# Kernel optimization log

Measured on AMD Instinct MI355X. Metric: run time of the kernel, lower is better.

## Reference

```python
import jax, jax.numpy as jnp
import numpy as np

DECAY = 0.95

def setup_inputs() -> dict:
    key = jax.random.key(0)
    k1, k2, k3, k4 = jax.random.split(key, 4)
    B, S, H, Dk, Dv = 4, 4096, 16, 64, 64
    return {
        "memory": jax.random.normal(k1, (H, Dk, Dv), dtype=jnp.float32),
        "keys": jax.random.normal(k2, (B, S, H, Dk), dtype=jnp.float32),
        "values": jax.random.normal(k3, (B, S, H, Dv), dtype=jnp.float32),
        "write_strengths": jax.random.uniform(k4, (B, S), dtype=jnp.float32),
    }

def reference(memory, keys, values, write_strengths):
    # M_new = decay * M + sum_{b,s} rho[b,s] * k[b,s,h] v[b,s,h]^T
    # Algebraically equivalent to per-head (rho-weighted) K^T V contraction;
    # avoids materializing the (B,S,H,Dk,Dv) outer-product tensor.
    delta = jnp.einsum('bs,bshk,bshv->hkv', write_strengths, keys, values)
    return DECAY * memory + delta
```

## Files before the change

kernel.cpp:

```cpp
#include <hip/hip_runtime.h>

constexpr int HH   = 16;
constexpr int DK   = 64;
constexpr int DV   = 64;
constexpr int ROWS = 16384;
constexpr int TS   = 32;
constexpr int NCHUNK = 64;
constexpr int RPC  = ROWS / NCHUNK;
constexpr int NT   = RPC / TS;
constexpr float DECAY = 0.95f;

__global__ __launch_bounds__(256) void init_out(const float* __restrict__ mem,
                                                float* __restrict__ out) {
    int i = blockIdx.x * blockDim.x + threadIdx.x;
    out[i] = DECAY * mem[i];
}

__global__ __launch_bounds__(256) void accum(const float* __restrict__ keys,
                                             const float* __restrict__ values,
                                             const float* __restrict__ rho,
                                             float* __restrict__ out) {
    __shared__ float sK[2][TS * DK];
    __shared__ float sV[2][TS * DV];

    const int t     = threadIdx.x;
    const int chunk = blockIdx.x;
    const int h     = blockIdx.y;

    const int tv = t & 15;
    const int tk = t >> 4;

    const int srow = t >> 4;
    const int sc4  = (t & 15) * 4;

    float acc[4][4] = {{0.f}};

    const int base_row = chunk * RPC;

    float4 kA, kB, vA, vB;

    {
        int rA = base_row + srow;
        int rB = rA + 16;
        kA = *(const float4*)(keys   + (rA * HH + h) * DK + sc4);
        kB = *(const float4*)(keys   + (rB * HH + h) * DK + sc4);
        vA = *(const float4*)(values + (rA * HH + h) * DV + sc4);
        vB = *(const float4*)(values + (rB * HH + h) * DV + sc4);
        float wA = rho[rA], wB = rho[rB];
        kA.x *= wA; kA.y *= wA; kA.z *= wA; kA.w *= wA;
        kB.x *= wB; kB.y *= wB; kB.z *= wB; kB.w *= wB;
        *(float4*)&sK[0][srow * DK + sc4]        = kA;
        *(float4*)&sK[0][(srow + 16) * DK + sc4] = kB;
        *(float4*)&sV[0][srow * DV + sc4]        = vA;
        *(float4*)&sV[0][(srow + 16) * DV + sc4] = vB;
    }
    __syncthreads();

    for (int tile = 0; tile < NT; ++tile) {
        const int cur  = tile & 1;
        const int nxt  = cur ^ 1;
        const bool more = (tile + 1) < NT;

        if (more) {
            int rA = base_row + (tile + 1) * TS + srow;
            int rB = rA + 16;
            kA = *(const float4*)(keys   + (rA * HH + h) * DK + sc4);
            kB = *(const float4*)(keys   + (rB * HH + h) * DK + sc4);
            vA = *(const float4*)(values + (rA * HH + h) * DV + sc4);
            vB = *(const float4*)(values + (rB * HH + h) * DV + sc4);
            float wA = rho[rA], wB = rho[rB];
            kA.x *= wA; kA.y *= wA; kA.z *= wA; kA.w *= wA;
            kB.x *= wB; kB.y *= wB; kB.z *= wB; kB.w *= wB;
        }

        const float* kb = sK[cur];
        const float* vb = sV[cur];
        #pragma unroll
        for (int s = 0; s < TS; ++s) {
            float4 kf = *(const float4*)(kb + s * DK + tk * 4);
            float4 vf = *(const float4*)(vb + s * DV + tv * 4);
            acc[0][0] = fmaf(kf.x, vf.x, acc[0][0]);
            acc[0][1] = fmaf(kf.x, vf.y, acc[0][1]);
            acc[0][2] = fmaf(kf.x, vf.z, acc[0][2]);
            acc[0][3] = fmaf(kf.x, vf.w, acc[0][3]);
            acc[1][0] = fmaf(kf.y, vf.x, acc[1][0]);
            acc[1][1] = fmaf(kf.y, vf.y, acc[1][1]);
            acc[1][2] = fmaf(kf.y, vf.z, acc[1][2]);
            acc[1][3] = fmaf(kf.y, vf.w, acc[1][3]);
            acc[2][0] = fmaf(kf.z, vf.x, acc[2][0]);
            acc[2][1] = fmaf(kf.z, vf.y, acc[2][1]);
            acc[2][2] = fmaf(kf.z, vf.z, acc[2][2]);
            acc[2][3] = fmaf(kf.z, vf.w, acc[2][3]);
            acc[3][0] = fmaf(kf.w, vf.x, acc[3][0]);
            acc[3][1] = fmaf(kf.w, vf.y, acc[3][1]);
            acc[3][2] = fmaf(kf.w, vf.z, acc[3][2]);
            acc[3][3] = fmaf(kf.w, vf.w, acc[3][3]);
        }
        __syncthreads();
        if (more) {
            *(float4*)&sK[nxt][srow * DK + sc4]        = kA;
            *(float4*)&sK[nxt][(srow + 16) * DK + sc4] = kB;
            *(float4*)&sV[nxt][srow * DV + sc4]        = vA;
            *(float4*)&sV[nxt][(srow + 16) * DV + sc4] = vB;
        }
        __syncthreads();
    }

    float* red = &sK[0][0];
    #pragma unroll
    for (int i = 0; i < 4; ++i)
        #pragma unroll
        for (int j = 0; j < 4; ++j)
            red[(tk * 4 + i) * DV + tv * 4 + j] = acc[i][j];
    __syncthreads();

    float* o = out + h * (DK * DV);
    #pragma unroll
    for (int i = 0; i < 16; ++i)
        atomicAdd(o + i * 256 + t, red[i * 256 + t]);
}

extern "C" void kernel_launch(void* const* d_in, const int* in_sizes, int n_in,
                              void* d_out, int out_size, void* d_ws, size_t ws_size,
                              hipStream_t stream) {
    const float* mem    = (const float*)d_in[0];
    const float* keys   = (const float*)d_in[1];
    const float* values = (const float*)d_in[2];
    const float* rho    = (const float*)d_in[3];
    float* out = (float*)d_out;

    init_out<<<dim3((HH * DK * DV) / 256), dim3(256), 0, stream>>>(mem, out);

    dim3 grid(NCHUNK, HH);
    accum<<<grid, dim3(256), 0, stream>>>(keys, values, rho, out);
}
```

Before: 164.7 us.

## Give each wavefront its own row slice with 8x8 register tiles

Each of the four wavefronts now handles a private quarter of the block's rows, with its own double-buffered LDS tiles. This removes the block-wide barriers from the main loop. Each thread now computes the full 64x64 outer product as an 8x8 register tile, which doubles FMAs per LDS load. The four per-wave partial sums are reduced in shared memory before the atomic adds. The cost is many more accumulator registers (64 per thread), and the new launch-bound hint could force spills.

```diff
diff --git a/kernel.cpp b/kernel.cpp
--- a/kernel.cpp
+++ b/kernel.cpp
@@ -1,123 +1,152 @@
 #include <hip/hip_runtime.h>
 
-constexpr int HH   = 16;
-constexpr int DK   = 64;
-constexpr int DV   = 64;
+
+constexpr int HH = 16;
+constexpr int DK = 64;
+constexpr int DV = 64;
 constexpr int ROWS = 16384;
-constexpr int TS   = 32;
 constexpr int NCHUNK = 64;
-constexpr int RPC  = ROWS / NCHUNK;
-constexpr int NT   = RPC / TS;
+constexpr int RPB = ROWS / NCHUNK;
+constexpr int RPW = RPB / 4;
+constexpr int TR = 8;
+constexpr int NT = RPW / TR;
 constexpr float DECAY = 0.95f;
 
 __global__ __launch_bounds__(256) void init_out(const float* __restrict__ mem,
                                                 float* __restrict__ out) {
-    int i = blockIdx.x * blockDim.x + threadIdx.x;
+    int i = blockIdx.x * 256 + threadIdx.x;
     out[i] = DECAY * mem[i];
 }
 
-__global__ __launch_bounds__(256) void accum(const float* __restrict__ keys,
-                                             const float* __restrict__ values,
-                                             const float* __restrict__ rho,
-                                             float* __restrict__ out) {
-    __shared__ float sK[2][TS * DK];
-    __shared__ float sV[2][TS * DV];
+__global__ __launch_bounds__(256, 4) void accum(const float* __restrict__ keys,
+                                                const float* __restrict__ values,
+                                                const float* __restrict__ rho,
+                                                float* __restrict__ out) {
+    __shared__ float smem[8192];
 
-    const int t     = threadIdx.x;
+    const int t    = threadIdx.x;
+    const int w    = t >> 6;
+    const int lane = t & 63;
+    const int tk   = lane >> 3;
+    const int tv   = lane & 7;
     const int chunk = blockIdx.x;
     const int h     = blockIdx.y;
 
-    const int tv = t & 15;
-    const int tk = t >> 4;
+    float* kb = smem + w * 1024;
+    float* vb = smem + 4096 + w * 1024;
 
-    const int srow = t >> 4;
-    const int sc4  = (t & 15) * 4;
+    const int row0 = chunk * RPB + w * RPW;
+    const int sr = lane >> 4;
+    const int sc = (lane & 15) * 4;
 
-    float acc[4][4] = {{0.f}};
+    float acc[8][8];
+    #pragma unroll
+    for (int i = 0; i < 8; ++i)
+        #pragma unroll
+        for (int j = 0; j < 8; ++j) acc[i][j] = 0.f;
 
-    const int base_row = chunk * RPC;
-
-    float4 kA, kB, vA, vB;
+    float4 kr0, kr1, vr0, vr1;
+    float w0, w1;
 
     {
-        int rA = base_row + srow;
-        int rB = rA + 16;
-        kA = *(const float4*)(keys   + (rA * HH + h) * DK + sc4);
-        kB = *(const float4*)(keys   + (rB * HH + h) * DK + sc4);
-        vA = *(const float4*)(values + (rA * HH + h) * DV + sc4);
-        vB = *(const float4*)(values + (rB * HH + h) * DV + sc4);
-        float wA = rho[rA], wB = rho[rB];
-        kA.x *= wA; kA.y *= wA; kA.z *= wA; kA.w *= wA;
-        kB.x *= wB; kB.y *= wB; kB.z *= wB; kB.w *= wB;
-        *(float4*)&sK[0][srow * DK + sc4]        = kA;
-        *(float4*)&sK[0][(srow + 16) * DK + sc4] = kB;
-        *(float4*)&sV[0][srow * DV + sc4]        = vA;
-        *(float4*)&sV[0][(srow + 16) * DV + sc4] = vB;
+        int r = row0;
+        const float* kp = keys   + ((r + sr) * HH + h) * DK + sc;
+        const float* vp = values + ((r + sr) * HH + h) * DV + sc;
+        kr0 = *(const float4*)kp;
+        kr1 = *(const float4*)(kp + 4 * HH * DK);
+        vr0 = *(const float4*)vp;
+        vr1 = *(const float4*)(vp + 4 * HH * DV);
+        w0 = rho[r + sr];
+        w1 = rho[r + sr + 4];
+        kr0.x *= w0; kr0.y *= w0; kr0.z *= w0; kr0.w *= w0;
+        kr1.x *= w1; kr1.y *= w1; kr1.z *= w1; kr1.w *= w1;
+        *(float4*)(kb + lane * 4)       = kr0;
+        *(float4*)(kb + 256 + lane * 4) = kr1;
+        *(float4*)(vb + lane * 4)       = vr0;
+        *(float4*)(vb + 256 + lane * 4) = vr1;
     }
-    __syncthreads();
 
     for (int tile = 0; tile < NT; ++tile) {
-        const int cur  = tile & 1;
-        const int nxt  = cur ^ 1;
+        const int cur = tile & 1;
+        const int nxt = cur ^ 1;
         const bool more = (tile + 1) < NT;
 
         if (more) {
-            int rA = base_row + (tile + 1) * TS + srow;
-            int rB = rA + 16;
-            kA = *(const float4*)(keys   + (rA * HH + h) * DK + sc4);
-            kB = *(const float4*)(keys   + (rB * HH + h) * DK + sc4);
-            vA = *(const float4*)(values + (rA * HH + h) * DV + sc4);
-            vB = *(const float4*)(values + (rB * HH + h) * DV + sc4);
-            float wA = rho[rA], wB = rho[rB];
-            kA.x *= wA; kA.y *= wA; kA.z *= wA; kA.w *= wA;
-            kB.x *= wB; kB.y *= wB; kB.z *= wB; kB.w *= wB;
+            int r = row0 + (tile + 1) * TR;
+            const float* kp = keys   + ((r + sr) * HH + h) * DK + sc;
+            const float* vp = values + ((r + sr) * HH + h) * DV + sc;
+            kr0 = *(const float4*)kp;
+            kr1 = *(const float4*)(kp + 4 * HH * DK);
+            vr0 = *(const float4*)vp;
+            vr1 = *(const float4*)(vp + 4 * HH * DV);
+            w0 = rho[r + sr];
+            w1 = rho[r + sr + 4];
         }
 
-        const float* kb = sK[cur];
-        const float* vb = sV[cur];
+        const float* kc = kb + cur * 512;
+        const float* vc = vb + cur * 512;
         #pragma unroll
-        for (int s = 0; s < TS; ++s) {
-            float4 kf = *(const float4*)(kb + s * DK + tk * 4);
-            float4 vf = *(const float4*)(vb + s * DV + tv * 4);
-            acc[0][0] = fmaf(kf.x, vf.x, acc[0][0]);
-            acc[0][1] = fmaf(kf.x, vf.y, acc[0][1]);
-            acc[0][2] = fmaf(kf.x, vf.z, acc[0][2]);
-            acc[0][3] = fmaf(kf.x, vf.w, acc[0][3]);
-            acc[1][0] = fmaf(kf.y, vf.x, acc[1][0]);
-            acc[1][1] = fmaf(kf.y, vf.y, acc[1][1]);
-            acc[1][2] = fmaf(kf.y, vf.z, acc[1][2]);
-            acc[1][3] = fmaf(kf.y, vf.w, acc[1][3]);
-            acc[2][0] = fmaf(kf.z, vf.x, acc[2][0]);
-            acc[2][1] = fmaf(kf.z, vf.y, acc[2][1]);
-            acc[2][2] = fmaf(kf.z, vf.z, acc[2][2]);
-            acc[2][3] = fmaf(kf.z, vf.w, acc[2][3]);
-            acc[3][0] = fmaf(kf.w, vf.x, acc[3][0]);
-            acc[3][1] = fmaf(kf.w, vf.y, acc[3][1]);
-            acc[3][2] = fmaf(kf.w, vf.z, acc[3][2]);
-            acc[3][3] = fmaf(kf.w, vf.w, acc[3][3]);
+        for (int s = 0; s < TR; ++s) {
+            float4 ka  = *(const float4*)(kc + s * 64 + tk * 8);
+            float4 ka2 = *(const float4*)(kc + s * 64 + tk * 8 + 4);
+            float4 va  = *(const float4*)(vc + s * 64 + tv * 8);
+            float4 va2 = *(const float4*)(vc + s * 64 + tv * 8 + 4);
+            float kv[8] = {ka.x, ka.y, ka.z, ka.w, ka2.x, ka2.y, ka2.z, ka2.w};
+            float vv[8] = {va.x, va.y, va.z, va.w, va2.x, va2.y, va2.z, va2.w};
+            #pragma unroll
+            for (int i = 0; i < 8; ++i)
+                #pragma unroll
+                for (int j = 0; j < 8; ++j)
+                    acc[i][j] = fmaf(kv[i], vv[j], acc[i][j]);
         }
-        __syncthreads();
+
         if (more) {
-            *(float4*)&sK[nxt][srow * DK + sc4]        = kA;
-            *(float4*)&sK[nxt][(srow + 16) * DK + sc4] = kB;
-            *(float4*)&sV[nxt][srow * DV + sc4]        = vA;
-            *(float4*)&sV[nxt][(srow + 16) * DV + sc4] = vB;
+            kr0.x *= w0; kr0.y *= w0; kr0.z *= w0; kr0.w *= w0;
+            kr1.x *= w1; kr1.y *= w1; kr1.z *= w1; kr1.w *= w1;
+            float* kn = kb + nxt * 512;
+            float* vn = vb + nxt * 512;
+            *(float4*)(kn + lane * 4)       = kr0;
+            *(float4*)(kn + 256 + lane * 4) = kr1;
+            *(float4*)(vn + lane * 4)       = vr0;
+            *(float4*)(vn + 256 + lane * 4) = vr1;
         }
-        __syncthreads();
     }
 
-    float* red = &sK[0][0];
-    #pragma unroll
-    for (int i = 0; i < 4; ++i)
+    __syncthreads();
+    float* red0 = smem;
+    float* red1 = smem + 4096;
+
+    if (w < 2) {
+        float* dst = (w == 0) ? red0 : red1;
         #pragma unroll
-        for (int j = 0; j < 4; ++j)
-            red[(tk * 4 + i) * DV + tv * 4 + j] = acc[i][j];
+        for (int i = 0; i < 8; ++i) {
+            float4 a0 = {acc[i][0], acc[i][1], acc[i][2], acc[i][3]};
+            float4 a1 = {acc[i][4], acc[i][5], acc[i][6], acc[i][7]};
+            *(float4*)(dst + (tk * 8 + i) * 64 + tv * 8)     = a0;
+            *(float4*)(dst + (tk * 8 + i) * 64 + tv * 8 + 4) = a1;
+        }
+    }
+    __syncthreads();
+    if (w >= 2) {
+        float* dst = (w == 2) ? red0 : red1;
+        #pragma unroll
+        for (int i = 0; i < 8; ++i) {
+            float4* p0 = (float4*)(dst + (tk * 8 + i) * 64 + tv * 8);
+            float4* p1 = p0 + 1;
+            float4 c0 = *p0, c1 = *p1;
+            c0.x += acc[i][0]; c0.y += acc[i][1]; c0.z += acc[i][2]; c0.w += acc[i][3];
+            c1.x += acc[i][4]; c1.y += acc[i][5]; c1.z += acc[i][6]; c1.w += acc[i][7];
+            *p0 = c0; *p1 = c1;
+        }
+    }
     __syncthreads();
 
     float* o = out + h * (DK * DV);
     #pragma unroll
-    for (int i = 0; i < 16; ++i)
-        atomicAdd(o + i * 256 + t, red[i * 256 + t]);
+    for (int i = 0; i < 16; ++i) {
+        int idx = i * 256 + t;
+        atomicAdd(o + idx, red0[idx] + red1[idx]);
+    }
 }
 
 extern "C" void kernel_launch(void* const* d_in, const int* in_sizes, int n_in,
```

Result: slower. 168.2 us (+2.1%).
